# Kernel optimization log

Measured on AMD Instinct MI355X. Metric: run time of the kernel, lower is better.

## Reference

```python
import jax, jax.numpy as jnp
import numpy as np

NUM_ITERATIONS = 3
LN_EPS = 1e-5


def setup_inputs() -> dict:
    key = jax.random.key(0)
    ks = jax.random.split(key, 10)
    B, L, Lv, H = 8, 2048, 256, 1024
    s = 1.0 / np.sqrt(H)
    s2 = 1.0 / np.sqrt(2 * H)
    return {
        "text_feat": jax.random.normal(ks[0], (B, L, H), dtype=jnp.float32),
        "vision_feat": jax.random.normal(ks[1], (B, Lv, H), dtype=jnp.float32),
        "Wt": jax.random.uniform(ks[2], (H, H), jnp.float32, -s, s),
        "bt": jax.random.uniform(ks[3], (H,), jnp.float32, -s, s),
        "Wv": jax.random.uniform(ks[4], (H, H), jnp.float32, -s, s),
        "bv": jax.random.uniform(ks[5], (H,), jnp.float32, -s, s),
        "Wg": jax.random.uniform(ks[6], (H, 2 * H), jnp.float32, -s2, s2),
        "bg": jax.random.uniform(ks[7], (H,), jnp.float32, -s2, s2),
        "gamma": jnp.ones((H,), jnp.float32),
        "beta": jnp.zeros((H,), jnp.float32),
    }


def reference(text_feat, vision_feat, Wt, bt, Wv, bv, Wg, bg, gamma, beta):
    B, L, H = text_feat.shape
    # mean-pool vision over its sequence, broadcast over L
    vision_pooled = jnp.mean(vision_feat, axis=1, keepdims=True)          # [B,1,H]
    text_proj = jnp.einsum('blh,oh->blo', text_feat, Wt) + bt             # [B,L,H]
    vision_proj = jnp.einsum('bkh,oh->bko', vision_pooled, Wv) + bv       # [B,1,H]
    vision_proj = jnp.broadcast_to(vision_proj, (B, L, H))                # expand to [B,L,H]

    # agreement is loop-invariant in the original code; compute once
    agreement = jnp.sum(text_proj * vision_proj, axis=-1, keepdims=True)  # [B,L,1]

    coupling = jnp.zeros((B, L, 1), dtype=text_feat.dtype)
    fused = text_feat
    for _ in range(NUM_ITERATIONS):
        routing_weights = jax.nn.softmax(coupling, axis=1)                # softmax over L
        weighted_vision = routing_weights * vision_proj                   # [B,L,H]
        # gate = sigmoid(Linear(concat(text_proj, weighted_vision)))
        Wg_t, Wg_v = Wg[:, :H], Wg[:, H:]
        gate_pre = (jnp.einsum('blh,oh->blo', text_proj, Wg_t)
                    + jnp.einsum('blh,oh->blo', weighted_vision, Wg_v) + bg)
        gate = jax.nn.sigmoid(gate_pre)
        fused = text_feat + gate * weighted_vision
        coupling = coupling + agreement

    # LayerNorm over last dim (dropout is identity in eval)
    mu = jnp.mean(fused, axis=-1, keepdims=True)
    var = jnp.mean(jnp.square(fused - mu), axis=-1, keepdims=True)
    out = (fused - mu) / jnp.sqrt(var + LN_EPS) * gamma + beta
    return out
```

## Files before the change

### kernel.cpp

```cpp
#include <hip/hip_runtime.h>
#include <hip/hip_bf16.h>
#include <hip/hip_fp8.h>

typedef __bf16 bf16_t;
typedef bf16_t bf16x4 __attribute__((ext_vector_type(4)));
typedef bf16_t bf16x8 __attribute__((ext_vector_type(8)));
typedef float  f32x4  __attribute__((ext_vector_type(4)));

#define B_  8
#define L_  2048
#define H_  1024
#define LV_ 256

typedef const __attribute__((address_space(1))) void* gptr_as1;
typedef __attribute__((address_space(3))) void* lptr_as3;

__device__ __forceinline__ void gload_lds16(void* lds_base, const void* gsrc) {
  __builtin_amdgcn_global_load_lds((gptr_as1)gsrc, (lptr_as3)lds_base, 16, 0, 0);
}
__device__ __forceinline__ void gload_lds4(void* lds_base, const void* gsrc) {
  __builtin_amdgcn_global_load_lds((gptr_as1)gsrc, (lptr_as3)lds_base, 4, 0, 0);
}

__device__ __forceinline__ unsigned char to_fp8(float x) {
  return __hip_fp8_e4m3(x).__x;
}

__global__ __launch_bounds__(256) void prep1(const float* __restrict__ vf,
                                             const float* __restrict__ Wt,
                                             const float* __restrict__ Wg,
                                             const float* __restrict__ bt,
                                             const float* __restrict__ bg,
                                             float* __restrict__ pooled,
                                             bf16_t* __restrict__ WtT,
                                             float* __restrict__ cbb,
                                             float* __restrict__ u) {
  __shared__ __align__(16) char shm[16640];
  int bid = blockIdx.x;
  int t = threadIdx.x;
  if (bid < 64) {
    float* part = (float*)shm;
    int b = bid >> 3, hc = bid & 7;
    int h = hc * 128 + (t & 127);
    int kh = t >> 7;
    const float* p = vf + (long)b * (LV_ * H_) + (long)kh * 128 * H_ + h;
    float s = 0.f;
    #pragma unroll 4
    for (int k = 0; k < 128; ++k) s += p[k * H_];
    part[t] = s;
    __syncthreads();
    if (t < 128)
      pooled[b * H_ + hc * 128 + t] = (part[t] + part[t + 128]) * (1.f / 256.f);
  } else if (bid < 320) {
    float (*tile)[65] = (float(*)[65])shm;
    int lb = bid - 64;
    int hr = (lb >> 4) * 64;
    int ec = (lb & 15) * 64;
    int lr = t >> 4, lc = t & 15;
    #pragma unroll
    for (int rr = 0; rr < 4; ++rr) {
      int r = rr * 16 + lr;
      float4 v = *(const float4*)(Wt + (long)(hr + r) * H_ + ec + lc * 4);
      tile[r][lc * 4 + 0] = v.x; tile[r][lc * 4 + 1] = v.y;
      tile[r][lc * 4 + 2] = v.z; tile[r][lc * 4 + 3] = v.w;
    }
    __syncthreads();
    #pragma unroll
    for (int rr = 0; rr < 4; ++rr) {
      int er = rr * 16 + lr;
      bf16x4 o = { (bf16_t)tile[lc * 4 + 0][er], (bf16_t)tile[lc * 4 + 1][er],
                   (bf16_t)tile[lc * 4 + 2][er], (bf16_t)tile[lc * 4 + 3][er] };
      *(bf16x4*)(WtT + (long)(ec + er) * H_ + hr + lc * 4) = o;
    }
  } else if (bid < 576) {
    int lb = bid - 320;
    int wid = t >> 6, lane = t & 63;
    int o = lb * 4 + wid;
    const float* wr = Wg + (long)o * 2048;
    float acc = 0.f;
    for (int j = 0; j < 16; ++j) acc += wr[lane + 64 * j] * bt[lane + 64 * j];
    for (int off = 32; off; off >>= 1) acc += __shfl_down(acc, off);
    if (lane == 0) cbb[o] = acc + bg[o];
  } else {
    int z = bid - 576;
    *(float4*)(u + z * 1024 + t * 4) = (float4){0.f, 0.f, 0.f, 0.f};
  }
}

__global__ void matvec8(const float* __restrict__ W, int ldw, int woff,
                        const float* __restrict__ x,
                        const float* __restrict__ bias,
                        float* __restrict__ out) {
  int wid = threadIdx.x >> 6, lane = threadIdx.x & 63;
  int o = blockIdx.x * 4 + wid;
  const float* wr = W + (long)o * ldw + woff;
  float acc[B_];
  #pragma unroll
  for (int b = 0; b < B_; ++b) acc[b] = 0.f;
  for (int j = 0; j < 16; ++j) {
    float w = wr[lane + 64 * j];
    #pragma unroll
    for (int b = 0; b < B_; ++b) acc[b] += w * x[b * H_ + lane + 64 * j];
  }
  #pragma unroll
  for (int b = 0; b < B_; ++b)
    for (int off = 32; off; off >>= 1) acc[b] += __shfl_down(acc[b], off);
  if (lane == 0) {
    float bb = bias ? bias[o] : 0.f;
    #pragma unroll
    for (int b = 0; b < B_; ++b) out[b * H_ + o] = acc[b] + bb;
  }
}

__global__ __launch_bounds__(256) void prep3(const float* __restrict__ Wg,
                                             const float* __restrict__ Wt,
                                             const float* __restrict__ vp,
                                             float* __restrict__ gv,
                                             float* __restrict__ u) {
  int bid = blockIdx.x;
  int t = threadIdx.x;
  if (bid < 256) {
    int wid = t >> 6, lane = t & 63;
    int o = bid * 4 + wid;
    const float* wr = Wg + (long)o * 2048 + 1024;
    float acc[B_];
    #pragma unroll
    for (int b = 0; b < B_; ++b) acc[b] = 0.f;
    for (int j = 0; j < 16; ++j) {
      float w = wr[lane + 64 * j];
      #pragma unroll
      for (int b = 0; b < B_; ++b) acc[b] += w * vp[b * H_ + lane + 64 * j];
    }
    #pragma unroll
    for (int b = 0; b < B_; ++b)
      for (int off = 32; off; off >>= 1) acc[b] += __shfl_down(acc[b], off);
    if (lane == 0) {
      #pragma unroll
      for (int b = 0; b < B_; ++b) gv[b * H_ + o] = acc[b];
    }
  } else {
    int lb = bid - 256;
    int e = (lb & 3) * 256 + t;
    int oc = lb >> 2;
    float a[B_];
    #pragma unroll
    for (int b = 0; b < B_; ++b) a[b] = 0.f;
    #pragma unroll
    for (int i = 0; i < 16; ++i) {
      int o = oc * 16 + i;
      float w = Wt[(long)o * H_ + e];
      #pragma unroll
      for (int b = 0; b < B_; ++b) a[b] += w * vp[b * H_ + o];
    }
    #pragma unroll
    for (int b = 0; b < B_; ++b) atomicAdd(u + b * 1024 + e, a[b]);
  }
}

__global__ __launch_bounds__(256) void cvt_wc(const float* __restrict__ text,
                                              const float* __restrict__ u,
                                              const float* __restrict__ Wg,
                                              const bf16_t* __restrict__ Bt,
                                              unsigned char* __restrict__ t8p,
                                              float* __restrict__ agr,
                                              unsigned char* __restrict__ Cw8) {
  __shared__ __align__(16) char shm[32800];
  int bid = blockIdx.x;
  int t = threadIdx.x;
  if (bid < 1024) {
    unsigned char (*q8)[1032] = (unsigned char(*)[1032])shm;
    float (*dred)[16] = (float(*)[16])(shm + 16512);
    int b = bid >> 7;
    int wid = t >> 6, lane = t & 63;
    const float4* trow = (const float4*)(text + (long)bid * (16 * H_));
    float4 uu = ((const float4*)(u + b * H_))[t];
    #pragma unroll 4
    for (int i = 0; i < 16; ++i) {
      float4 v = trow[i * 256 + t];
      float d = v.x * uu.x + v.y * uu.y + v.z * uu.z + v.w * uu.w;
      for (int off = 32; off; off >>= 1) d += __shfl_down(d, off);
      if (!lane) dred[wid][i] = d;
      uchar4 q = { to_fp8(v.x), to_fp8(v.y), to_fp8(v.z), to_fp8(v.w) };
      *(uchar4*)&q8[i][t * 4] = q;
    }
    __syncthreads();
    if (t < 16)
      agr[bid * 16 + t] = dred[0][t] + dred[1][t] + dred[2][t] + dred[3][t];
    unsigned char* dst = t8p + (long)bid * 16384;
    #pragma unroll
    for (int c = 0; c < 8; ++c) {
      int kb = wid * 8 + c;
      uint2 r = *(const uint2*)&q8[lane & 15][kb * 32 + (lane >> 4) * 8];
      *(uint2*)(dst + kb * 512 + lane * 8) = r;
    }
    return;
  }
  const int tid = t;
  const int wid = tid >> 6, lane = tid & 63;
  const int fr = lane & 15, fkb = (lane >> 4) * 16, fq = (lane >> 4) * 4;
  const int wm = wid >> 1, wn = wid & 1;
  const int lb = bid - 1024;
  const int tm = lb & 15, tn = lb >> 4;
  const int m0 = tm * 64, n0 = tn * 64;

  char* ldsA = shm;
  float* red = (float*)(shm + 32768);
  (void)red;

  const int d0 = tid * 16;
  const int p  = d0 ^ (((d0 >> 7) & 7) << 4);
  const int rS = p >> 7, cS = (p & 127) >> 1;

  const int swz = (fr & 7) << 4;
  const int e0 = fkb ^ swz;
  const int e1 = (64 + fkb) ^ swz;

  auto stage = [&](int tt) {
    char* base = ldsA + (tt & 1) * 16384;
    gload_lds16(base + 8192 + d0,        Bt + (long)(n0 + rS) * H_ + tt * 64 + cS);
    gload_lds16(base + 8192 + 4096 + d0, Bt + (long)(n0 + 32 + rS) * H_ + tt * 64 + cS);
    const float* a0 = Wg + (long)(m0 + rS) * 2048 + tt * 64 + cS;
    const float* a1 = Wg + (long)(m0 + 32 + rS) * 2048 + tt * 64 + cS;
    float4 x0 = *(const float4*)a0, x1 = *(const float4*)(a0 + 4);
    float4 y0 = *(const float4*)a1, y1 = *(const float4*)(a1 + 4);
    bf16x8 bx = { (bf16_t)x0.x, (bf16_t)x0.y, (bf16_t)x0.z, (bf16_t)x0.w,
                  (bf16_t)x1.x, (bf16_t)x1.y, (bf16_t)x1.z, (bf16_t)x1.w };
    bf16x8 by = { (bf16_t)y0.x, (bf16_t)y0.y, (bf16_t)y0.z, (bf16_t)y0.w,
                  (bf16_t)y1.x, (bf16_t)y1.y, (bf16_t)y1.z, (bf16_t)y1.w };
    *(bf16x8*)(base + d0) = bx;
    *(bf16x8*)(base + 4096 + d0) = by;
  };

  f32x4 acc[2][2];
  #pragma unroll
  for (int m = 0; m < 2; ++m)
    #pragma unroll
    for (int n = 0; n < 2; ++n) acc[m][n] = (f32x4){0.f, 0.f, 0.f, 0.f};

  stage(0);
  __syncthreads();
  for (int tt = 0; tt < 16; ++tt) {
    if (tt + 1 < 16) stage(tt + 1);
    char* buf = ldsA + (tt & 1) * 16384;
    char* AR = buf + (wm * 32 + fr) * 128;
    char* BR = buf + 8192 + (wn * 32 + fr) * 128;
    bf16x8 a[2][2], b[2][2];
    #pragma unroll
    for (int m = 0; m < 2; ++m) {
      a[m][0] = *(const bf16x8*)(AR + m * 2048 + e0);
      a[m][1] = *(const bf16x8*)(AR + m * 2048 + e1);
      b[m][0] = *(const bf16x8*)(BR + m * 2048 + e0);
      b[m][1] = *(const bf16x8*)(BR + m * 2048 + e1);
    }
    #pragma unroll
    for (int m = 0; m < 2; ++m)
      #pragma unroll
      for (int n = 0; n < 2; ++n) {
        acc[m][n] = __builtin_amdgcn_mfma_f32_16x16x32_bf16(a[m][0], b[n][0], acc[m][n], 0, 0, 0);
        acc[m][n] = __builtin_amdgcn_mfma_f32_16x16x32_bf16(a[m][1], b[n][1], acc[m][n], 0, 0, 0);
      }
    __syncthreads();
  }
  #pragma unroll
  for (int m = 0; m < 2; ++m)
    #pragma unroll
    for (int r_ = 0; r_ < 4; ++r_) {
      int row = m0 + wm * 32 + m * 16 + fq + r_;
      #pragma unroll
      for (int n = 0; n < 2; ++n) {
        int col = n0 + wn * 32 + n * 16 + fr;
        Cw8[((row >> 4) * 32 + (col >> 5)) * 512
            + ((row & 15) + (((col >> 3) & 3) << 4)) * 8 + (col & 7)]
          = to_fp8(acc[m][n][r_] * 16.f);
      }
    }
}

#define BOFF 16777216
__global__ __launch_bounds__(512, 2)
void gemm_ln(const unsigned char* __restrict__ AB,
             const float* __restrict__ textf,
             const float* __restrict__ cbb, const float* __restrict__ agrb,
             const float* __restrict__ gvb, const float* __restrict__ vpb,
             const float* __restrict__ gamma, const float* __restrict__ beta,
             float* __restrict__ out) {
  extern __shared__ __align__(16) char dlds[];
  const int tid  = threadIdx.x;
  const int w    = tid >> 6;
  const int lane = tid & 63;
  const int fr   = lane & 15;
  const int fq   = (lane >> 4) * 4;
  const int bid  = blockIdx.x;
  const long m0  = (long)bid * 64;
  const int bat  = (int)(m0 >> 11);

  {
    float* red = (float*)(dlds + 124928);
    float* rvA = (float*)(dlds + 124992);
    float4 av = *(const float4*)(agrb + (long)bat * 2048 + tid * 4);
    float mloc = fmaxf(fmaxf(av.x, av.y), fmaxf(av.z, av.w)) * 2.f;
    #pragma unroll
    for (int off = 32; off; off >>= 1) mloc = fmaxf(mloc, __shfl_xor(mloc, off));
    if ((tid & 63) == 0) red[tid >> 6] = mloc;
    __syncthreads();
    float mx = red[0];
    #pragma unroll
    for (int i = 1; i < 8; ++i) mx = fmaxf(mx, red[i]);
    float sl = __expf(2.f * av.x - mx) + __expf(2.f * av.y - mx)
             + __expf(2.f * av.z - mx) + __expf(2.f * av.w - mx);
    #pragma unroll
    for (int off = 32; off; off >>= 1) sl += __shfl_xor(sl, off);
    __syncthreads();
    if ((tid & 63) == 0) red[tid >> 6] = sl;
    __syncthreads();
    float ssum = red[0] + red[1] + red[2] + red[3]
               + red[4] + red[5] + red[6] + red[7];
    if (tid < 64) rvA[tid] = __expf(2.f * agrb[m0 + tid] - mx) / ssum;
    __syncthreads();
  }

  const int o0 = tid * 4;
  const unsigned char* aSrc = AB + (long)bid * 65536 + (o0 >> 9) * 16384 + (o0 & 511);
  const unsigned char* bSrc = AB + BOFF + (long)(tid >> 5) * 16384 + (tid & 31) * 16;
  const int bD = (tid >> 5) * 512 + (tid & 31) * 16;

  {
    char* P = dlds + 104448;
    if (tid < 256) {
      gload_lds16(P + tid * 16,          cbb + tid * 4);
      gload_lds16(P + 8192 + tid * 16,   vpb + bat * H_ + tid * 4);
      gload_lds16(P + 16384 + tid * 16,  beta + tid * 4);
    } else {
      int t2 = tid - 256;
      gload_lds16(P + 4096 + t2 * 16,    gvb + bat * H_ + t2 * 4);
      gload_lds16(P + 12288 + t2 * 16,   gamma + t2 * 4);
    }
  }

  f32x4 acc[4][8];
  #pragma unroll
  for (int m = 0; m < 4; ++m)
    #pragma unroll
    for (int n = 0; n < 8; ++n) acc[m][n] = (f32x4){0.f, 0.f, 0.f, 0.f};

#define STAGE(t)                                                        \
  {                                                                     \
    gload_lds4(dlds + ((t) % 3) * 2048 + o0, aSrc + (t) * 512);         \
    _Pragma("unroll")                                                   \
    for (int r_ = 0; r_ < 4; ++r_)                                      \
      gload_lds16(dlds + 6144 + ((t) % 3) * 32768 + r_ * 8192 + bD,     \
                  bSrc + (long)r_ * 262144 + (t) * 512);                \
  }
#define KITER(t, WN)                                                    \
  {                                                                     \
    __builtin_amdgcn_sched_barrier(0);                                  \
    asm volatile("s_waitcnt vmcnt(" #WN ")" ::: "memory");              \
    __builtin_amdgcn_s_barrier();                                       \
    __builtin_amdgcn_sched_barrier(0);                                  \
    if ((t) + 2 < 32) STAGE((t) + 2)                                    \
    const char* Ab_ = dlds + ((t) % 3) * 2048 + lane * 8;               \
    const char* Bb_ = dlds + 6144 + ((t) % 3) * 32768 + w * 4096        \
                           + lane * 8;                                  \
    long a_[4], b_[8];                                                  \
    _Pragma("unroll")                                                   \
    for (int m_ = 0; m_ < 4; ++m_)                                      \
      a_[m_] = *(const long*)(Ab_ + m_ * 512);                          \
    _Pragma("unroll")                                                   \
    for (int n_ = 0; n_ < 8; ++n_)                                      \
      b_[n_] = *(const long*)(Bb_ + n_ * 512);                          \
    _Pragma("unroll")                                                   \
    for (int m_ = 0; m_ < 4; ++m_)                                      \
      _Pragma("unroll")                                                 \
      for (int n_ = 0; n_ < 8; ++n_)                                    \
        acc[m_][n_] = __builtin_amdgcn_mfma_f32_16x16x32_fp8_fp8(       \
            a_[m_], b_[n_], acc[m_][n_], 0, 0, 0);                      \
  }

  STAGE(0)
  asm volatile("" ::: "memory");
  STAGE(1)

  KITER(0, 5)  KITER(1, 5)  KITER(2, 5)  KITER(3, 5)
  KITER(4, 5)  KITER(5, 5)  KITER(6, 5)  KITER(7, 5)
  KITER(8, 5)  KITER(9, 5)  KITER(10, 5) KITER(11, 5)
  KITER(12, 5) KITER(13, 5) KITER(14, 5) KITER(15, 5)
  KITER(16, 5) KITER(17, 5) KITER(18, 5) KITER(19, 5)
  KITER(20, 5) KITER(21, 5) KITER(22, 5) KITER(23, 5)
  KITER(24, 5) KITER(25, 5) KITER(26, 5) KITER(27, 5)
  KITER(28, 5) KITER(29, 5) KITER(30, 5) KITER(31, 0)
#undef KITER
#undef STAGE

  const int lr = tid >> 5;
  const int jj = tid & 31;
  char* P = dlds + 104448;
  const float* rvA = (const float*)(dlds + 124992);

  #pragma unroll
  for (int m = 0; m < 4; ++m) {
    __syncthreads();
    #pragma unroll
    for (int n = 0; n < 8; ++n) {
      #pragma unroll
      for (int r = 0; r < 4; ++r) {
        int rl = fq + r;
        int c  = (w * 128 + n * 16 + fr) ^ (((rl >> 2) & 3) << 4);
        *(float*)(dlds + rl * 4096 + c * 4) = acc[m][n][r];
      }
    }
    __syncthreads();
    long row = m0 + m * 16 + lr;
    float rv = rvA[m * 16 + lr];
    const float* tf = textf + row * H_;
    const int rot = ((lr >> 2) & 3) << 4;
    float s = 0.f, q = 0.f;
    #pragma unroll 2
    for (int k = 0; k < 8; ++k) {
      int c0 = k * 128 + jj * 4;
      char* slot = dlds + lr * 4096 + ((c0 ^ rot) * 4);
      f32x4 a4 = *(const f32x4*)slot;
      float4 t4  = *(const float4*)(tf + c0);
      f32x4 cb4 = *(const f32x4*)(P + c0 * 4);
      f32x4 gv4 = *(const f32x4*)(P + 4096 + c0 * 4);
      f32x4 vp4 = *(const f32x4*)(P + 8192 + c0 * 4);
      f32x4 f4;
      float gp, g;
      gp = a4[0] * 0.0625f + cb4[0] + rv * gv4[0];
      g = 1.f / (1.f + __expf(-gp));
      f4[0] = t4.x + g * rv * vp4[0];
      gp = a4[1] * 0.0625f + cb4[1] + rv * gv4[1];
      g = 1.f / (1.f + __expf(-gp));
      f4[1] = t4.y + g * rv * vp4[1];
      gp = a4[2] * 0.0625f + cb4[2] + rv * gv4[2];
      g = 1.f / (1.f + __expf(-gp));
      f4[2] = t4.z + g * rv * vp4[2];
      gp = a4[3] * 0.0625f + cb4[3] + rv * gv4[3];
      g = 1.f / (1.f + __expf(-gp));
      f4[3] = t4.w + g * rv * vp4[3];
      *(f32x4*)slot = f4;
      s += f4[0] + f4[1] + f4[2] + f4[3];
      q += f4[0] * f4[0] + f4[1] * f4[1] + f4[2] * f4[2] + f4[3] * f4[3];
    }
    #pragma unroll
    for (int off = 1; off < 32; off <<= 1) {
      s += __shfl_xor(s, off);
      q += __shfl_xor(q, off);
    }
    float mu  = s * (1.f / H_);
    float var = q * (1.f / H_) - mu * mu;
    float inv = rsqrtf(var + 1e-5f);
    float* op = out + row * H_;
    #pragma unroll 2
    for (int k = 0; k < 8; ++k) {
      int c0 = k * 128 + jj * 4;
      f32x4 f4 = *(const f32x4*)(dlds + lr * 4096 + ((c0 ^ rot) * 4));
      f32x4 gg = *(const f32x4*)(P + 12288 + c0 * 4);
      f32x4 bb = *(const f32x4*)(P + 16384 + c0 * 4);
      float4 o4;
      o4.x = (f4[0] - mu) * inv * gg[0] + bb[0];
      o4.y = (f4[1] - mu) * inv * gg[1] + bb[1];
      o4.z = (f4[2] - mu) * inv * gg[2] + bb[2];
      o4.w = (f4[3] - mu) * inv * gg[3] + bb[3];
      *(float4*)(op + c0) = o4;
    }
  }
}

extern "C" void kernel_launch(void* const* d_in, const int* in_sizes, int n_in,
                              void* d_out, int out_size, void* d_ws, size_t ws_size,
                              hipStream_t stream) {
  const float* text  = (const float*)d_in[0];
  const float* vis   = (const float*)d_in[1];
  const float* Wt    = (const float*)d_in[2];
  const float* bt    = (const float*)d_in[3];
  const float* Wv    = (const float*)d_in[4];
  const float* bv    = (const float*)d_in[5];
  const float* Wg    = (const float*)d_in[6];
  const float* bg    = (const float*)d_in[7];
  const float* gamma = (const float*)d_in[8];
  const float* beta  = (const float*)d_in[9];
  float* out = (float*)d_out;

  char* ws = (char*)d_ws;
  unsigned char* t8p   = (unsigned char*)(ws);
  unsigned char* Wc8p  = (unsigned char*)(ws + (size_t)16777216);
  bf16_t* WtT_b = (bf16_t*)(ws + (size_t)17825792);
  float*  pooled = (float*)(ws + (size_t)19922944);
  float*  vp     = (float*)(ws + (size_t)19955712);
  float*  gv     = (float*)(ws + (size_t)19988480);
  float*  u      = (float*)(ws + (size_t)20021248);
  float*  cbb    = (float*)(ws + (size_t)20054016);
  float*  agr    = (float*)(ws + (size_t)20123648);

  static bool smem_set = false;
  if (!smem_set) {
    (void)hipFuncSetAttribute((const void*)gemm_ln,
                              hipFuncAttributeMaxDynamicSharedMemorySize, 125440);
    smem_set = true;
  }

  prep1<<<584, 256, 0, stream>>>(vis, Wt, Wg, bt, bg, pooled, WtT_b, cbb, u);
  matvec8<<<256, 256, 0, stream>>>(Wv, 1024, 0, pooled, bv, vp);
  prep3<<<512, 256, 0, stream>>>(Wg, Wt, vp, gv, u);
  cvt_wc<<<1280, 256, 0, stream>>>(text, u, Wg, WtT_b, t8p, agr, Wc8p);
  gemm_ln<<<256, 512, 125440, stream>>>(t8p, text, cbb, agr, gv, vp,
                                        gamma, beta, out);
}
```

Baseline: 99.93 us.

## Give each wave private double-buffered LDS tiles and drop block barriers in GEMM

```diff
diff --git a/kernel.cpp b/kernel.cpp
--- a/kernel.cpp
+++ b/kernel.cpp
@@ -17,9 +17,6 @@
 
 __device__ __forceinline__ void gload_lds16(void* lds_base, const void* gsrc) {
   __builtin_amdgcn_global_load_lds((gptr_as1)gsrc, (lptr_as3)lds_base, 16, 0, 0);
-}
-__device__ __forceinline__ void gload_lds4(void* lds_base, const void* gsrc) {
-  __builtin_amdgcn_global_load_lds((gptr_as1)gsrc, (lptr_as3)lds_base, 4, 0, 0);
 }
 
 __device__ __forceinline__ unsigned char to_fp8(float x) {
@@ -186,12 +183,12 @@
     __syncthreads();
     if (t < 16)
       agr[bid * 16 + t] = dred[0][t] + dred[1][t] + dred[2][t] + dred[3][t];
-    unsigned char* dst = t8p + (long)bid * 16384;
+    unsigned char* dst = t8p + (long)(bid >> 2) * 65536 + (bid & 3) * 512;
     #pragma unroll
     for (int c = 0; c < 8; ++c) {
       int kb = wid * 8 + c;
       uint2 r = *(const uint2*)&q8[lane & 15][kb * 32 + (lane >> 4) * 8];
-      *(uint2*)(dst + kb * 512 + lane * 8) = r;
+      *(uint2*)(dst + kb * 2048 + lane * 8) = r;
     }
     return;
   }
@@ -204,8 +201,6 @@
   const int m0 = tm * 64, n0 = tn * 64;
 
   char* ldsA = shm;
-  float* red = (float*)(shm + 32768);
-  (void)red;
 
   const int d0 = tid * 16;
   const int p  = d0 ^ (((d0 >> 7) & 7) << 4);
@@ -269,7 +264,7 @@
       #pragma unroll
       for (int n = 0; n < 2; ++n) {
         int col = n0 + wn * 32 + n * 16 + fr;
-        Cw8[((row >> 4) * 32 + (col >> 5)) * 512
+        Cw8[(long)(row >> 7) * 131072 + (col >> 5) * 4096 + ((row >> 4) & 7) * 512
             + ((row & 15) + (((col >> 3) & 3) << 4)) * 8 + (col & 7)]
           = to_fp8(acc[m][n][r_] * 16.f);
       }
@@ -295,8 +290,8 @@
   const int bat  = (int)(m0 >> 11);
 
   {
-    float* red = (float*)(dlds + 124928);
-    float* rvA = (float*)(dlds + 124992);
+    float* red = (float*)(dlds + 118784);
+    float* rvA = (float*)(dlds + 118848);
     float4 av = *(const float4*)(agrb + (long)bat * 2048 + tid * 4);
     float mloc = fmaxf(fmaxf(av.x, av.y), fmaxf(av.z, av.w)) * 2.f;
     #pragma unroll
@@ -319,13 +314,8 @@
     __syncthreads();
   }
 
-  const int o0 = tid * 4;
-  const unsigned char* aSrc = AB + (long)bid * 65536 + (o0 >> 9) * 16384 + (o0 & 511);
-  const unsigned char* bSrc = AB + BOFF + (long)(tid >> 5) * 16384 + (tid & 31) * 16;
-  const int bD = (tid >> 5) * 512 + (tid & 31) * 16;
-
   {
-    char* P = dlds + 104448;
+    char* P = dlds + 98304;
     if (tid < 256) {
       gload_lds16(P + tid * 16,          cbb + tid * 4);
       gload_lds16(P + 8192 + tid * 16,   vpb + bat * H_ + tid * 4);
@@ -337,6 +327,10 @@
     }
   }
 
+  const unsigned char* aSrc = AB + (long)bid * 65536 + lane * 16;
+  const unsigned char* bSrc = AB + BOFF + (long)w * 131072 + lane * 16;
+  char* const wBase = dlds + w * 12288;
+
   f32x4 acc[4][8];
   #pragma unroll
   for (int m = 0; m < 4; ++m)
@@ -345,29 +339,30 @@
 
 #define STAGE(t)                                                        \
   {                                                                     \
-    gload_lds4(dlds + ((t) % 3) * 2048 + o0, aSrc + (t) * 512);         \
+    char* D_ = wBase + ((t) & 1) * 6144 + lane * 16;                    \
+    const unsigned char* As_ = aSrc + (t) * 2048;                       \
+    gload_lds16(D_,        As_);                                        \
+    gload_lds16(D_ + 1024, As_ + 1024);                                 \
+    const unsigned char* Bs_ = bSrc + (t) * 4096;                       \
     _Pragma("unroll")                                                   \
     for (int r_ = 0; r_ < 4; ++r_)                                      \
-      gload_lds16(dlds + 6144 + ((t) % 3) * 32768 + r_ * 8192 + bD,     \
-                  bSrc + (long)r_ * 262144 + (t) * 512);                \
+      gload_lds16(D_ + 2048 + r_ * 1024, Bs_ + r_ * 1024);              \
   }
 #define KITER(t, WN)                                                    \
   {                                                                     \
+    asm volatile("s_waitcnt lgkmcnt(0)" ::: "memory");                  \
     __builtin_amdgcn_sched_barrier(0);                                  \
+    if ((t) + 1 < 32) STAGE((t) + 1)                                    \
     asm volatile("s_waitcnt vmcnt(" #WN ")" ::: "memory");              \
-    __builtin_amdgcn_s_barrier();                                       \
     __builtin_amdgcn_sched_barrier(0);                                  \
-    if ((t) + 2 < 32) STAGE((t) + 2)                                    \
-    const char* Ab_ = dlds + ((t) % 3) * 2048 + lane * 8;               \
-    const char* Bb_ = dlds + 6144 + ((t) % 3) * 32768 + w * 4096        \
-                           + lane * 8;                                  \
+    const char* R_ = wBase + ((t) & 1) * 6144 + lane * 8;               \
     long a_[4], b_[8];                                                  \
     _Pragma("unroll")                                                   \
     for (int m_ = 0; m_ < 4; ++m_)                                      \
-      a_[m_] = *(const long*)(Ab_ + m_ * 512);                          \
+      a_[m_] = *(const long*)(R_ + m_ * 512);                           \
     _Pragma("unroll")                                                   \
     for (int n_ = 0; n_ < 8; ++n_)                                      \
-      b_[n_] = *(const long*)(Bb_ + n_ * 512);                          \
+      b_[n_] = *(const long*)(R_ + 2048 + n_ * 512);                    \
     _Pragma("unroll")                                                   \
     for (int m_ = 0; m_ < 4; ++m_)                                      \
       _Pragma("unroll")                                                 \
@@ -377,24 +372,22 @@
   }
 
   STAGE(0)
-  asm volatile("" ::: "memory");
-  STAGE(1)
-
-  KITER(0, 5)  KITER(1, 5)  KITER(2, 5)  KITER(3, 5)
-  KITER(4, 5)  KITER(5, 5)  KITER(6, 5)  KITER(7, 5)
-  KITER(8, 5)  KITER(9, 5)  KITER(10, 5) KITER(11, 5)
-  KITER(12, 5) KITER(13, 5) KITER(14, 5) KITER(15, 5)
-  KITER(16, 5) KITER(17, 5) KITER(18, 5) KITER(19, 5)
-  KITER(20, 5) KITER(21, 5) KITER(22, 5) KITER(23, 5)
-  KITER(24, 5) KITER(25, 5) KITER(26, 5) KITER(27, 5)
-  KITER(28, 5) KITER(29, 5) KITER(30, 5) KITER(31, 0)
+
+  KITER(0, 6)  KITER(1, 6)  KITER(2, 6)  KITER(3, 6)
+  KITER(4, 6)  KITER(5, 6)  KITER(6, 6)  KITER(7, 6)
+  KITER(8, 6)  KITER(9, 6)  KITER(10, 6) KITER(11, 6)
+  KITER(12, 6) KITER(13, 6) KITER(14, 6) KITER(15, 6)
+  KITER(16, 6) KITER(17, 6) KITER(18, 6) KITER(19, 6)
+  KITER(20, 6) KITER(21, 6) KITER(22, 6) KITER(23, 6)
+  KITER(24, 6) KITER(25, 6) KITER(26, 6) KITER(27, 6)
+  KITER(28, 6) KITER(29, 6) KITER(30, 6) KITER(31, 0)
 #undef KITER
 #undef STAGE
 
   const int lr = tid >> 5;
   const int jj = tid & 31;
-  char* P = dlds + 104448;
-  const float* rvA = (const float*)(dlds + 124992);
+  char* P = dlds + 98304;
+  const float* rvA = (const float*)(dlds + 118848);
 
   #pragma unroll
   for (int m = 0; m < 4; ++m) {
@@ -495,7 +488,7 @@
   static bool smem_set = false;
   if (!smem_set) {
     (void)hipFuncSetAttribute((const void*)gemm_ln,
-                              hipFuncAttributeMaxDynamicSharedMemorySize, 125440);
+                              hipFuncAttributeMaxDynamicSharedMemorySize, 119296);
     smem_set = true;
   }
 
@@ -503,6 +496,6 @@
   matvec8<<<256, 256, 0, stream>>>(Wv, 1024, 0, pooled, bv, vp);
   prep3<<<512, 256, 0, stream>>>(Wg, Wt, vp, gv, u);
   cvt_wc<<<1280, 256, 0, stream>>>(text, u, Wg, WtT_b, t8p, agr, Wc8p);
-  gemm_ln<<<256, 512, 125440, stream>>>(t8p, text, cbb, agr, gv, vp,
+  gemm_ln<<<256, 512, 119296, stream>>>(t8p, text, cbb, agr, gv, vp,
                                         gamma, beta, out);
 }
```

New measurement: 98.89 us. No clear change (-1.0%).
